# Kernel tuning notes

Measured on AMD Instinct MI355X. Metric: run time of the kernel, lower is better.

## Reference

```python
import jax, jax.numpy as jnp
import numpy as np

B, T, D, H, O, L = 32, 512, 512, 512, 2, 2


def setup_inputs() -> dict:
    key = jax.random.key(0)
    ks = jax.random.split(key, 8)
    s_in = 1.0 / np.sqrt(D + H)
    s_h = 1.0 / np.sqrt(H + H)
    x = jax.random.normal(ks[0], (B, T, D), dtype=jnp.float32)
    # Fused gate weights per layer: columns ordered [forget | input | candidate | output]
    W0 = jax.random.uniform(ks[1], (D + H, 4 * H), jnp.float32, -s_in, s_in)
    b0 = jax.random.uniform(ks[2], (4 * H,), jnp.float32, -s_in, s_in)
    W1 = jax.random.uniform(ks[3], (H + H, 4 * H), jnp.float32, -s_h, s_h)
    b1 = jax.random.uniform(ks[4], (4 * H,), jnp.float32, -s_h, s_h)
    s_r = 1.0 / np.sqrt(H)
    Wr = jax.random.uniform(ks[5], (H, O), jnp.float32, -s_r, s_r)
    br = jax.random.uniform(ks[6], (O,), jnp.float32, -s_r, s_r)
    return {"x": x, "W0": W0, "b0": b0, "W1": W1, "b1": b1, "Wr": Wr, "br": br}


def _lstm_cell(xt, h, c, W, b):
    # One fused GEMM for all 4 gates, then elementwise gate math.
    z = jnp.concatenate([xt, h], axis=1) @ W + b  # [B, 4H]
    f, i, g, o = jnp.split(z, 4, axis=1)
    new_c = c * jax.nn.sigmoid(f) + jnp.tanh(g) * jax.nn.sigmoid(i)
    # NB: original module applies tanh to the OLD cell state c (faithful to source).
    new_h = jax.nn.sigmoid(o) * jnp.tanh(c)
    return new_h, new_c


def reference(x, W0, b0, W1, b1, Wr, br):
    Bb = x.shape[0]
    zeros = jnp.zeros((Bb, H), dtype=x.dtype)

    def step(carry, xt):
        h1, c1, h2, c2 = carry
        nh1, nc1 = _lstm_cell(xt, h1, c1, W0, b0)
        nh2, nc2 = _lstm_cell(nh1, h2, c2, W1, b1)
        return (nh1, nc1, nh2, nc2), nh2

    _, ys = jax.lax.scan(step, (zeros, zeros, zeros, zeros), jnp.swapaxes(x, 0, 1))
    out = jnp.swapaxes(ys, 0, 1)  # [B, T, H]
    return out @ Wr + br  # [B, T, O]
```

## Files before the change

### kernel.cpp

```cpp
#include <hip/hip_runtime.h>
#include <hip/hip_bf16.h>
#include <stdint.h>

typedef unsigned short u16;
typedef unsigned int u32;
typedef unsigned long long u64;
typedef __attribute__((ext_vector_type(8))) short bf16x8;
typedef __attribute__((ext_vector_type(4))) float f32x4;
typedef __attribute__((ext_vector_type(4))) u32 u32x4;

#define TT 512
#define WPS ((size_t)2048 * 1024)
#define ZRS 8
#define HRS 16
#define HRS2 4

#define LD16C(dst, addr) asm volatile("global_load_dwordx4 %0, %1, off sc0 sc1" : "=v"(dst) : "v"(addr))
#define LD8C(dst, addr)  asm volatile("global_load_dwordx2 %0, %1, off sc0 sc1" : "=v"(dst) : "v"(addr))
#define LD4C(dst, addr)  asm volatile("global_load_dword %0, %1, off sc0 sc1"   : "=v"(dst) : "v"(addr))
#define ST4C(addr, v)    asm volatile("global_store_dword %0, %1, off sc0 sc1"  :: "v"(addr), "v"(v) : "memory")
#define ST8C(addr, v)    asm volatile("global_store_dwordx2 %0, %1, off sc0 sc1":: "v"(addr), "v"(v) : "memory")
#define ST16C(addr, v)   asm volatile("global_store_dwordx4 %0, %1, off sc0 sc1":: "v"(addr), "v"(v) : "memory")
#define VM0()            do { asm volatile("s_waitcnt vmcnt(0)" ::: "memory"); \
                              __builtin_amdgcn_sched_barrier(0); } while (0)

__device__ __forceinline__ u16 f2bf(float f) {
  u32 u = __builtin_bit_cast(u32, f);
  return (u16)((u + 0x7FFFu + ((u >> 16) & 1u)) >> 16);
}
__device__ __forceinline__ float bf2f(u16 h) {
  u32 u = ((u32)h) << 16;
  return __builtin_bit_cast(float, u);
}
__device__ __forceinline__ float sigm(float x) { return 1.0f / (1.0f + expf(-x)); }
__device__ __forceinline__ f32x4 mfma16(bf16x8 a, bf16x8 b, f32x4 c) {
  return __builtin_amdgcn_mfma_f32_16x16x32_bf16(a, b, c, 0, 0, 0);
}
__device__ __forceinline__ u32 cvtpk(float a, float b) {
  u32 r;
  asm volatile("v_cvt_pk_bf16_f32 %0, %1, %2" : "=v"(r) : "v"(a), "v"(b));
  return r;
}
__device__ __forceinline__ void mark_err(u32* err) {
  __hip_atomic_fetch_add(err, 1u, __ATOMIC_RELAXED, __HIP_MEMORY_SCOPE_AGENT);
}
__device__ __forceinline__ u64 pack3(float v, u32 tag) {
  u16 p0 = f2bf(v); float r1 = v - bf2f(p0);
  u16 p1 = f2bf(r1); u16 p2 = f2bf(r1 - bf2f(p1));
  return (u64)((u32)p0 | ((u32)p1 << 16)) | ((u64)((u32)p2 | (tag << 16)) << 32);
}
__device__ __forceinline__ float zval(u64 w) {
  return bf2f((u16)(w & 0xFFFFu)) + bf2f((u16)((w >> 16) & 0xFFFFu))
       + bf2f((u16)((w >> 32) & 0xFFFFu));
}

__device__ __forceinline__ void wait_slots(const u32* slots, int ln, u32 tgt,
                                           u32* lastv, int* bail, u32* err) {
  if (*bail) return;
  if (__ballot(*lastv < tgt) == 0ull) return;
  const u32* ptr = slots + (ln & 31);
  int n = 0;
  for (;;) {
    u32 v;
    LD4C(v, ptr);
    VM0();
    if (v > *lastv) *lastv = v;
    if (__ballot(*lastv < tgt) == 0ull) return;
    __builtin_amdgcn_s_sleep(2);
    if (++n > 400000) { *bail = 1; if (ln == 0) mark_err(err); return; }
  }
}

__device__ __forceinline__ void head_poll(const u64* p, u32 texp, u32* err) {
  int n = 0;
  for (;;) {
    u64 hw;
    LD8C(hw, p);
    VM0();
    if (__ballot((u32)(hw >> 48) != texp) == 0ull) return;
    __builtin_amdgcn_s_sleep(1);
    if (++n > 600000) { if ((threadIdx.x & 63) == 0) mark_err(err); return; }
  }
}

__global__ void prep_w(const float* __restrict__ W, u16* __restrict__ WT) {
  int i = blockIdx.x * 256 + threadIdx.x;
  if (i >= 2048 * 1024) return;
  int n = i >> 10, k = i & 1023;
  float v = W[(size_t)k * 2048 + n];
  u16 p0 = f2bf(v);  float r  = v - bf2f(p0);
  u16 p1 = f2bf(r);  float r2 = r - bf2f(p1);
  u16 p2 = f2bf(r2);
  size_t o = (size_t)n * 1024 + k;
  WT[o] = p0;
  WT[WPS + o] = p1;
  WT[2 * WPS + o] = p2;
}

template <int LAYER>
__device__ void chain(char* smem, int p, int bid,
                      const float* __restrict__ bias,
                      const u16* __restrict__ WT,
                      const u64* Zring, u64* hG,
                      const u32* progOther, u32* progSelf,
                      u16* h2hi, u32* err) {
  u16* wl = (u16*)smem;
  float* zl = (float*)(smem + 131072);
  const int tid = threadIdx.x;

#pragma unroll 1
  for (int it = 0; it < 32; ++it) {
    int id = it * 256 + tid;
    int pl = id >> 12, rem = id & 4095, rho = rem >> 6, m = rem & 63;
    int n = ((rho >> 4) << 9) + (bid << 4) + (rho & 15);
    u32x4 v = *(const u32x4*)(WT + (size_t)pl * WPS + (size_t)n * 1024 + 512 + m * 8);
    int dst = pl * 65536 + rho * 1024 + ((m << 4) ^ ((rho & 7) << 4));
    *(u32x4*)((char*)wl + dst) = v;
  }

  const int ln = tid & 63, kq = tid >> 6;
  const int fr = ln & 15, kg8 = (ln >> 4) << 3;
  const int row = tid >> 4, hc = tid & 15;
  float bsv[4];
#pragma unroll
  for (int g = 0; g < 4; ++g) bsv[g] = bias[(g << 9) + (bid << 4) + hc];
  const int ka = kq * 128 + kg8;
  const u16* w2base[4];
#pragma unroll
  for (int nt = 0; nt < 4; ++nt)
    w2base[nt] = WT + 2 * WPS + (size_t)((nt << 9) + (bid << 4) + fr) * 1024 + 512 + ka;
  const int hrm = (LAYER == 1) ? (HRS - 1) : (HRS2 - 1);

  float creg = 0.0f;
  u32 lastbp = 0;
  int bail = 0;
  __syncthreads();

#pragma unroll 1
  for (int t = 0; t < TT; ++t) {
    if (LAYER == 1 && kq == 0 && t >= HRS - 1)
      wait_slots(progOther, ln, (u32)(t - (HRS - 1)), &lastbp, &bail, err);

    const u64* hb = hG + (size_t)(t & hrm) * (16 * 512) + (size_t)fr * 512 + ka;
    const u64* zb = Zring + (size_t)(t & (ZRS - 1)) * (16 * 2048) + (size_t)row * 2048
                  + (bid << 4) + hc;
    const u32 texp = (u32)t, zexp = (u32)(t + 1);

    head_poll(hb, texp, err);

    u32x4 hv[4][4];
    u64 zw[4];
    int tries = 0;
    for (;;) {
#pragma unroll
      for (int kt = 0; kt < 4; ++kt)
#pragma unroll
        for (int j = 0; j < 4; ++j) LD16C(hv[kt][j], hb + kt * 32 + 2 * j);
#pragma unroll
      for (int g = 0; g < 4; ++g) LD8C(zw[g], zb + ((size_t)g << 9));
      VM0();
      u32 bad = 0;
#pragma unroll
      for (int kt = 0; kt < 4; ++kt)
#pragma unroll
        for (int j = 0; j < 4; ++j)
          bad |= ((hv[kt][j].y >> 16) ^ texp) | ((hv[kt][j].w >> 16) ^ texp);
#pragma unroll
      for (int g = 0; g < 4; ++g) bad |= ((u32)(zw[g] >> 48) ^ zexp);
      if (__ballot(bad != 0) == 0ull) break;
      if (++tries > 500000) { if (ln == 0) mark_err(err); break; }
      __builtin_amdgcn_s_sleep(1);
    }

    f32x4 acc[4] = {{0.f,0.f,0.f,0.f},{0.f,0.f,0.f,0.f},{0.f,0.f,0.f,0.f},{0.f,0.f,0.f,0.f}};
#pragma unroll
    for (int kt = 0; kt < 4; ++kt) {
      u32 r0[4], r1[4], r2[4];
#pragma unroll
      for (int j = 0; j < 4; ++j) {
        u32 lo0 = hv[kt][j].x, hi0 = hv[kt][j].y, lo1 = hv[kt][j].z, hi1 = hv[kt][j].w;
        r0[j] = (lo0 & 0xFFFFu) | (lo1 << 16);
        r1[j] = (lo0 >> 16) | (lo1 & 0xFFFF0000u);
        r2[j] = (hi0 & 0xFFFFu) | (hi1 << 16);
      }
      bf16x8 a0 = __builtin_bit_cast(bf16x8, *(u32x4*)r0);
      bf16x8 a1 = __builtin_bit_cast(bf16x8, *(u32x4*)r1);
      bf16x8 a2 = __builtin_bit_cast(bf16x8, *(u32x4*)r2);
#pragma unroll
      for (int nt = 0; nt < 4; ++nt) {
        int rho = (nt << 4) + fr;
        int kb = ((ka + kt * 32) << 1) ^ ((rho & 7) << 4);
        bf16x8 w0 = *(const bf16x8*)((char*)wl + rho * 1024 + kb);
        bf16x8 w1 = *(const bf16x8*)((char*)wl + 65536 + rho * 1024 + kb);
        bf16x8 w2 = *(const bf16x8*)(w2base[nt] + kt * 32);
        acc[nt] = mfma16(a0, w0, acc[nt]);
        acc[nt] = mfma16(a1, w0, acc[nt]);
        acc[nt] = mfma16(a2, w0, acc[nt]);
        acc[nt] = mfma16(a0, w1, acc[nt]);
        acc[nt] = mfma16(a1, w1, acc[nt]);
        acc[nt] = mfma16(a0, w2, acc[nt]);
      }
    }
    const int r4 = (ln >> 4) << 2;
    if (kq < 2) {
#pragma unroll
      for (int nt = 0; nt < 4; ++nt)
#pragma unroll
        for (int r = 0; r < 4; ++r)
          zl[(kq * 16 + r4 + r) * 66 + (nt << 4) + fr] = acc[nt][r];
    }
    __syncthreads();
    if (kq >= 2) {
#pragma unroll
      for (int nt = 0; nt < 4; ++nt)
#pragma unroll
        for (int r = 0; r < 4; ++r)
          zl[((kq - 2) * 16 + r4 + r) * 66 + (nt << 4) + fr] += acc[nt][r];
    }
    __syncthreads();

    float z4[4];
#pragma unroll
    for (int g = 0; g < 4; ++g)
      z4[g] = zl[row * 66 + (g << 4) + hc] + zl[(16 + row) * 66 + (g << 4) + hc]
            + zval(zw[g]) + bsv[g];
    float sf = sigm(z4[0]);
    float si = sigm(z4[1]);
    float tg = tanhf(z4[2]);
    float so = sigm(z4[3]);
    float hn = so * tanhf(creg);
    creg = creg * sf + tg * si;
    u64 word = pack3(hn, (u32)(t + 1));
    size_t ho = (size_t)((t + 1) & hrm) * (16 * 512) + (size_t)row * 512 + (bid << 4) + hc;
    ST8C(hG + ho, word);
    if (LAYER == 2)
      h2hi[(size_t)(t + 1) * 16384 + (size_t)(p * 16 + row) * 512 + (bid << 4) + hc] =
          (u16)(word & 0xFFFFu);
    __syncthreads();
    if (tid == 0) ST4C(progSelf + bid, (u32)(t + 1));
  }
}

__device__ void worker(char* smem, int w, const float* __restrict__ x,
                       const u16* __restrict__ W0T, const u16* __restrict__ W1T,
                       const u64* h1G, u64* Z0R, u64* ZcR,
                       const u32* prog1, const u32* prog2, u32* err) {
  const int s = w & 63, q = w >> 6;
  u16* wl1 = (u16*)smem;
  u16* wl0 = (u16*)(smem + 65536);
  float* zl = (float*)(smem + 131072);
  const int tid = threadIdx.x;

#pragma unroll 1
  for (int it = 0; it < 32; ++it) {
    int id = it * 256 + tid;
    int sl = id >> 12, rem = id & 4095, pl = rem >> 11, rem2 = rem & 2047;
    int rho = rem2 >> 6, m = rem2 & 63;
    const u16* WT = sl ? W0T : W1T;
    u32x4 v = *(const u32x4*)(WT + (size_t)pl * WPS + (size_t)(32 * s + rho) * 1024 + m * 8);
    int dst = sl * 65536 + pl * 32768 + rho * 1024 + ((m << 4) ^ ((rho & 7) << 4));
    *(u32x4*)((char*)wl1 + dst) = v;
  }

  const int ln = tid & 63, kq = tid >> 6;
  const int fr = ln & 15, kg8 = (ln >> 4) << 3;
  const int row = tid >> 4, c2 = (tid & 15) * 2;
  const int ka = kq * 128 + kg8;
  u32 last1[2] = {0, 0}, last2[2] = {0, 0}, lastbp[2] = {0, 0};
  int bail = 0;
  __syncthreads();

#pragma unroll 1
  for (int k = 0;; ++k) {
    int t = 2 * k + q;
    if (t > 511) break;

    int nz = (k < 3) ? 2 : 1;
#pragma unroll 1
    for (int e = 0; e < nz; ++e) {
      int tz = (e == 0 && k < 3) ? t : t + 6;
      if (tz > 511) continue;
#pragma unroll 1
      for (int p = 0; p < 2; ++p) {
        if (kq == 0 && tz >= ZRS)
          wait_slots(prog1 + p * 32, ln, (u32)(tz - ZRS + 1), &lastbp[p], &bail, err);
        const float* xb = x + (size_t)(p * 16 + fr) * TT * 512 + (size_t)tz * 512 + ka;
        f32x4 acc[2] = {{0.f,0.f,0.f,0.f},{0.f,0.f,0.f,0.f}};
#pragma unroll
        for (int kt = 0; kt < 4; ++kt) {
          f32x4 f0 = *(const f32x4*)(xb + kt * 32);
          f32x4 f1 = *(const f32x4*)(xb + kt * 32 + 4);
          u32 r0[4], r1[4], r2[4];
#pragma unroll
          for (int j = 0; j < 4; ++j) {
            float v0 = (j < 2) ? f0[j * 2] : f1[(j - 2) * 2];
            float v1 = (j < 2) ? f0[j * 2 + 1] : f1[(j - 2) * 2 + 1];
            u32 pk0 = cvtpk(v0, v1);
            float h0 = __builtin_bit_cast(float, pk0 << 16);
            float h1f = __builtin_bit_cast(float, pk0 & 0xFFFF0000u);
            float q0 = v0 - h0, q1 = v1 - h1f;
            u32 pk1 = cvtpk(q0, q1);
            float g0 = __builtin_bit_cast(float, pk1 << 16);
            float g1 = __builtin_bit_cast(float, pk1 & 0xFFFF0000u);
            u32 s0 = __builtin_bit_cast(u32, q0 - g0);
            u32 s1 = __builtin_bit_cast(u32, q1 - g1);
            r0[j] = pk0; r1[j] = pk1;
            r2[j] = (s0 >> 16) | (s1 & 0xFFFF0000u);
          }
          bf16x8 a0 = __builtin_bit_cast(bf16x8, *(u32x4*)r0);
          bf16x8 a1 = __builtin_bit_cast(bf16x8, *(u32x4*)r1);
          bf16x8 a2 = __builtin_bit_cast(bf16x8, *(u32x4*)r2);
#pragma unroll
          for (int nt = 0; nt < 2; ++nt) {
            int rho = (nt << 4) + fr;
            int kb = ((ka + kt * 32) << 1) ^ ((rho & 7) << 4);
            bf16x8 w0 = *(const bf16x8*)((char*)wl0 + rho * 1024 + kb);
            bf16x8 w1 = *(const bf16x8*)((char*)wl0 + 32768 + rho * 1024 + kb);
            bf16x8 w2 = *(const bf16x8*)(W0T + 2 * WPS + (size_t)(32 * s + rho) * 1024 + ka + kt * 32);
            acc[nt] = mfma16(a0, w0, acc[nt]);
            acc[nt] = mfma16(a1, w0, acc[nt]);
            acc[nt] = mfma16(a2, w0, acc[nt]);
            acc[nt] = mfma16(a0, w1, acc[nt]);
            acc[nt] = mfma16(a1, w1, acc[nt]);
            acc[nt] = mfma16(a0, w2, acc[nt]);
          }
        }
        const int r4 = (ln >> 4) << 2;
        if (kq < 2) {
#pragma unroll
          for (int nt = 0; nt < 2; ++nt)
#pragma unroll
            for (int r = 0; r < 4; ++r)
              zl[(kq * 16 + r4 + r) * 34 + (nt << 4) + fr] = acc[nt][r];
        }
        __syncthreads();
        if (kq >= 2) {
#pragma unroll
          for (int nt = 0; nt < 2; ++nt)
#pragma unroll
            for (int r = 0; r < 4; ++r)
              zl[((kq - 2) * 16 + r4 + r) * 34 + (nt << 4) + fr] += acc[nt][r];
        }
        __syncthreads();
        float v0 = zl[row * 34 + c2] + zl[(16 + row) * 34 + c2];
        float v1 = zl[row * 34 + c2 + 1] + zl[(16 + row) * 34 + c2 + 1];
        u64 w0 = pack3(v0, (u32)(tz + 1));
        u64 w1 = pack3(v1, (u32)(tz + 1));
        u32x4 st = { (u32)w0, (u32)(w0 >> 32), (u32)w1, (u32)(w1 >> 32) };
        u64* dst = Z0R + (size_t)p * ZRS * 16 * 2048 + (size_t)(tz & (ZRS - 1)) * (16 * 2048)
                 + (size_t)row * 2048 + 32 * s + c2;
        ST16C(dst, st);
        __syncthreads();
      }
    }

#pragma unroll 1
    for (int p = 0; p < 2; ++p) {
      if (kq == 0 && t >= ZRS)
        wait_slots(prog2 + p * 32, ln, (u32)(t - ZRS + 1), &last2[p], &bail, err);
      const u64* hb = h1G + (size_t)p * HRS * 16 * 512
                    + (size_t)((t + 1) & (HRS - 1)) * (16 * 512) + (size_t)fr * 512 + ka;
      const u32 texp = (u32)(t + 1);
      head_poll(hb, texp, err);
      u32x4 hv[4][4];
      int tries = 0;
      for (;;) {
#pragma unroll
        for (int kt = 0; kt < 4; ++kt)
#pragma unroll
          for (int j = 0; j < 4; ++j) LD16C(hv[kt][j], hb + kt * 32 + 2 * j);
        VM0();
        u32 bad = 0;
#pragma unroll
        for (int kt = 0; kt < 4; ++kt)
#pragma unroll
          for (int j = 0; j < 4; ++j)
            bad |= ((hv[kt][j].y >> 16) ^ texp) | ((hv[kt][j].w >> 16) ^ texp);
        if (__ballot(bad != 0) == 0ull) break;
        if (++tries > 500000) { if (ln == 0) mark_err(err); break; }
        __builtin_amdgcn_s_sleep(1);
      }
      f32x4 acc[2] = {{0.f,0.f,0.f,0.f},{0.f,0.f,0.f,0.f}};
#pragma unroll
      for (int kt = 0; kt < 4; ++kt) {
        u32 r0[4], r1[4], r2[4];
#pragma unroll
        for (int j = 0; j < 4; ++j) {
          u32 lo0 = hv[kt][j].x, hi0 = hv[kt][j].y, lo1 = hv[kt][j].z, hi1 = hv[kt][j].w;
          r0[j] = (lo0 & 0xFFFFu) | (lo1 << 16);
          r1[j] = (lo0 >> 16) | (lo1 & 0xFFFF0000u);
          r2[j] = (hi0 & 0xFFFFu) | (hi1 << 16);
        }
        bf16x8 a0 = __builtin_bit_cast(bf16x8, *(u32x4*)r0);
        bf16x8 a1 = __builtin_bit_cast(bf16x8, *(u32x4*)r1);
        bf16x8 a2 = __builtin_bit_cast(bf16x8, *(u32x4*)r2);
#pragma unroll
        for (int nt = 0; nt < 2; ++nt) {
          int rho = (nt << 4) + fr;
          int kb = ((ka + kt * 32) << 1) ^ ((rho & 7) << 4);
          bf16x8 w0 = *(const bf16x8*)((char*)wl1 + rho * 1024 + kb);
          bf16x8 w1 = *(const bf16x8*)((char*)wl1 + 32768 + rho * 1024 + kb);
          bf16x8 w2 = *(const bf16x8*)(W1T + 2 * WPS + (size_t)(32 * s + rho) * 1024 + ka + kt * 32);
          acc[nt] = mfma16(a0, w0, acc[nt]);
          acc[nt] = mfma16(a1, w0, acc[nt]);
          acc[nt] = mfma16(a2, w0, acc[nt]);
          acc[nt] = mfma16(a0, w1, acc[nt]);
          acc[nt] = mfma16(a1, w1, acc[nt]);
          acc[nt] = mfma16(a0, w2, acc[nt]);
        }
      }
      const int r4 = (ln >> 4) << 2;
      if (kq < 2) {
#pragma unroll
        for (int nt = 0; nt < 2; ++nt)
#pragma unroll
          for (int r = 0; r < 4; ++r)
            zl[(kq * 16 + r4 + r) * 34 + (nt << 4) + fr] = acc[nt][r];
      }
      __syncthreads();
      if (kq >= 2) {
#pragma unroll
        for (int nt = 0; nt < 2; ++nt)
#pragma unroll
          for (int r = 0; r < 4; ++r)
            zl[((kq - 2) * 16 + r4 + r) * 34 + (nt << 4) + fr] += acc[nt][r];
      }
      __syncthreads();
      float v0 = zl[row * 34 + c2] + zl[(16 + row) * 34 + c2];
      float v1 = zl[row * 34 + c2 + 1] + zl[(16 + row) * 34 + c2 + 1];
      u64 w0 = pack3(v0, (u32)(t + 1));
      u64 w1 = pack3(v1, (u32)(t + 1));
      u32x4 st = { (u32)w0, (u32)(w0 >> 32), (u32)w1, (u32)(w1 >> 32) };
      u64* dst = ZcR + (size_t)p * ZRS * 16 * 2048 + (size_t)(t & (ZRS - 1)) * (16 * 2048)
               + (size_t)row * 2048 + 32 * s + c2;
      ST16C(dst, st);
      __syncthreads();
    }
  }
}

__global__ void __launch_bounds__(256, 1) mega(
    const float* __restrict__ x,
    const float* __restrict__ bias0, const float* __restrict__ bias1,
    const u16* __restrict__ W0T, const u16* __restrict__ W1T,
    u64* Z0R, u64* ZcR, u64* h1G, u64* h2G, u16* h2hi, u32* flags) {
  __shared__ char smem[139520];
  const int blk = blockIdx.x;
  const int r8 = blk & 7, g8 = blk >> 3;
  u32* prog1 = flags;
  u32* prog2 = flags + 64;
  u32* err = flags + 128;
  if (r8 < 2) {
    int p = r8;
    chain<1>(smem, p, g8, bias0, W0T,
             Z0R + (size_t)p * ZRS * 16 * 2048, h1G + (size_t)p * HRS * 16 * 512,
             prog2 + p * 32, prog1 + p * 32, nullptr, err);
  } else if (r8 < 4) {
    int p = r8 - 2;
    chain<2>(smem, p, g8, bias1, W1T,
             ZcR + (size_t)p * ZRS * 16 * 2048, h2G + (size_t)p * HRS2 * 16 * 512,
             nullptr, prog2 + p * 32, h2hi, err);
  } else {
    worker(smem, (r8 - 4) * 32 + g8, x, W0T, W1T, h1G, Z0R, ZcR, prog1, prog2, err);
  }
}

__global__ void proj(const u16* __restrict__ y,
                     const float* __restrict__ Wr, const float* __restrict__ br,
                     float* __restrict__ out) {
  int gw = (blockIdx.x * blockDim.x + threadIdx.x) >> 6;
  int ln = threadIdx.x & 63;
  int t = gw >> 5, b = gw & 31;
  const u16* yp = y + (size_t)(t + 1) * 16384 + (size_t)b * 512 + ln * 8;
  u32x4 v = *(const u32x4*)yp;
  float p0 = 0.f, p1 = 0.f;
#pragma unroll
  for (int jj = 0; jj < 8; ++jj) {
    u16 hh = (u16)((v[jj >> 1] >> ((jj & 1) * 16)) & 0xFFFFu);
    float yv = bf2f(hh);
    int j = ln * 8 + jj;
    p0 += yv * Wr[j * 2 + 0];
    p1 += yv * Wr[j * 2 + 1];
  }
#pragma unroll
  for (int o = 32; o; o >>= 1) { p0 += __shfl_down(p0, o, 64); p1 += __shfl_down(p1, o, 64); }
  if (ln == 0) {
    out[((size_t)b * 512 + t) * 2 + 0] = p0 + br[0];
    out[((size_t)b * 512 + t) * 2 + 1] = p1 + br[1];
  }
}

__global__ void fail_mark(float* out, float code) {
  if (threadIdx.x == 0 && blockIdx.x == 0) out[0] = code;
}
__global__ void err_check(const u32* flags, float* out) {
  if (threadIdx.x == 0 && blockIdx.x == 0) {
    u32 e = flags[128];
    if (e) out[0] = 1.0e6f + (float)e;
  }
}

extern "C" void kernel_launch(void* const* d_in, const int* in_sizes, int n_in,
                              void* d_out, int out_size, void* d_ws, size_t ws_size,
                              hipStream_t stream) {
  (void)in_sizes; (void)n_in; (void)out_size;
  const float* x  = (const float*)d_in[0];
  const float* W0 = (const float*)d_in[1];
  const float* b0 = (const float*)d_in[2];
  const float* W1 = (const float*)d_in[3];
  const float* b1 = (const float*)d_in[4];
  const float* Wr = (const float*)d_in[5];
  const float* br = (const float*)d_in[6];
  float* out = (float*)d_out;

  char* ws = (char*)d_ws;
  size_t off = 0;
  auto take = [&](size_t n) { char* p = ws + off; off = (off + n + 255) & ~(size_t)255; return p; };

  u16* W0T  = (u16*)take(3 * WPS * 2);
  u16* W1T  = (u16*)take(3 * WPS * 2);
  u64* Z0R  = (u64*)take((size_t)2 * ZRS * 16 * 2048 * 8);
  u64* ZcR  = (u64*)take((size_t)2 * ZRS * 16 * 2048 * 8);
  u64* h1G  = (u64*)take((size_t)2 * HRS * 16 * 512 * 8);
  u64* h2G  = (u64*)take((size_t)2 * HRS2 * 16 * 512 * 8);
  u16* h2hi = (u16*)take((size_t)513 * 16384 * 2);
  u32* flags = (u32*)take(129 * 4);

  if (off > ws_size) {
    fail_mark<<<1, 1, 0, stream>>>(out, 2.0e6f);
    return;
  }

  hipMemsetAsync(flags, 0, 129 * 4, stream);
  hipMemsetAsync(Z0R, 0, (size_t)2 * ZRS * 16 * 2048 * 8, stream);
  hipMemsetAsync(ZcR, 0, (size_t)2 * ZRS * 16 * 2048 * 8, stream);
  hipMemsetAsync(h1G, 0, (size_t)2 * HRS * 16 * 512 * 8, stream);
  hipMemsetAsync(h2G, 0, (size_t)2 * HRS2 * 16 * 512 * 8, stream);

  prep_w<<<8192, 256, 0, stream>>>(W0, W0T);
  prep_w<<<8192, 256, 0, stream>>>(W1, W1T);
  (void)hipGetLastError();
  mega<<<256, 256, 0, stream>>>(x, b0, b1, W0T, W1T, Z0R, ZcR, h1G, h2G, h2hi, flags);
  if (hipGetLastError() != hipSuccess) {
    fail_mark<<<1, 1, 0, stream>>>(out, 3.0e6f);
    return;
  }
  proj<<<4096, 256, 0, stream>>>(h2hi, Wr, br, out);
  err_check<<<1, 1, 0, stream>>>(flags, out);
}
```

Baseline: 4.047 ms.

## Add XCD-local hidden-state mirror with device-scope fallback and defer Z polling

Each chain block now writes its hidden state twice: once with a device-scope store and once with an sc0-only store into a separate mirror buffer. Chain blocks in the same group poll and load from the mirror using sc0 loads, which are intended to be served from the shared L2 of the XCD instead of going device-wide. If the mirror poll times out they fall back to the device-scope copy. The Z ring load is issued before the h poll and its tag check is deferred until after the MMA reduction, taking it off the critical path. The risks are an extra store per step, correctness that depends on all blocks of a chain landing on the same XCD (the fallback handles the other case), and more complex polling logic.

```diff
diff --git a/kernel.cpp b/kernel.cpp
--- a/kernel.cpp
+++ b/kernel.cpp
@@ -18,9 +18,12 @@
 #define LD16C(dst, addr) asm volatile("global_load_dwordx4 %0, %1, off sc0 sc1" : "=v"(dst) : "v"(addr))
 #define LD8C(dst, addr)  asm volatile("global_load_dwordx2 %0, %1, off sc0 sc1" : "=v"(dst) : "v"(addr))
 #define LD4C(dst, addr)  asm volatile("global_load_dword %0, %1, off sc0 sc1"   : "=v"(dst) : "v"(addr))
+#define LD16L(dst, addr) asm volatile("global_load_dwordx4 %0, %1, off sc0"     : "=v"(dst) : "v"(addr))
+#define LD8L(dst, addr)  asm volatile("global_load_dwordx2 %0, %1, off sc0"     : "=v"(dst) : "v"(addr))
 #define ST4C(addr, v)    asm volatile("global_store_dword %0, %1, off sc0 sc1"  :: "v"(addr), "v"(v) : "memory")
 #define ST8C(addr, v)    asm volatile("global_store_dwordx2 %0, %1, off sc0 sc1":: "v"(addr), "v"(v) : "memory")
 #define ST16C(addr, v)   asm volatile("global_store_dwordx4 %0, %1, off sc0 sc1":: "v"(addr), "v"(v) : "memory")
+#define ST8L(addr, v)    asm volatile("global_store_dwordx2 %0, %1, off"        :: "v"(addr), "v"(v) : "memory")
 #define VM0()            do { asm volatile("s_waitcnt vmcnt(0)" ::: "memory"); \
                               __builtin_amdgcn_sched_barrier(0); } while (0)
 
@@ -101,7 +104,7 @@
 __device__ void chain(char* smem, int p, int bid,
                       const float* __restrict__ bias,
                       const u16* __restrict__ WT,
-                      const u64* Zring, u64* hG,
+                      const u64* Zring, u64* hL, u64* hG,
                       const u32* progOther, u32* progSelf,
                       u16* h2hi, u32* err) {
   u16* wl = (u16*)smem;
@@ -130,10 +133,12 @@
   for (int nt = 0; nt < 4; ++nt)
     w2base[nt] = WT + 2 * WPS + (size_t)((nt << 9) + (bid << 4) + fr) * 1024 + 512 + ka;
   const int hrm = (LAYER == 1) ? (HRS - 1) : (HRS2 - 1);
+  const int pcol = ((ln >> 1) << 4) + ((ln & 1) << 9);
 
   float creg = 0.0f;
   u32 lastbp = 0;
   int bail = 0;
+  int useG = 0;
   __syncthreads();
 
 #pragma unroll 1
@@ -141,23 +146,44 @@
     if (LAYER == 1 && kq == 0 && t >= HRS - 1)
       wait_slots(progOther, ln, (u32)(t - (HRS - 1)), &lastbp, &bail, err);
 
-    const u64* hb = hG + (size_t)(t & hrm) * (16 * 512) + (size_t)fr * 512 + ka;
+    const size_t soff = (size_t)(t & hrm) * (16 * 512);
+    const u64* hbL = hL + soff + (size_t)fr * 512 + ka;
+    const u64* hbG = hG + soff + (size_t)fr * 512 + ka;
     const u64* zb = Zring + (size_t)(t & (ZRS - 1)) * (16 * 2048) + (size_t)row * 2048
                   + (bid << 4) + hc;
     const u32 texp = (u32)t, zexp = (u32)(t + 1);
 
-    head_poll(hb, texp, err);
+    u64 zw[4];
+#pragma unroll
+    for (int g = 0; g < 4; ++g) LD8C(zw[g], zb + ((size_t)g << 9));
+
+    if (!useG) {
+      int n = 0;
+      for (;;) {
+        u64 hw;
+        LD8L(hw, hL + soff + pcol);
+        VM0();
+        if (__ballot((u32)(hw >> 48) != texp) == 0ull) break;
+        __builtin_amdgcn_s_sleep(1);
+        if (++n > 4000) { useG = 1; break; }
+      }
+    }
+    if (useG) head_poll(hG + soff + pcol, texp, err);
 
     u32x4 hv[4][4];
-    u64 zw[4];
     int tries = 0;
     for (;;) {
-#pragma unroll
-      for (int kt = 0; kt < 4; ++kt)
-#pragma unroll
-        for (int j = 0; j < 4; ++j) LD16C(hv[kt][j], hb + kt * 32 + 2 * j);
-#pragma unroll
-      for (int g = 0; g < 4; ++g) LD8C(zw[g], zb + ((size_t)g << 9));
+      if (!useG) {
+#pragma unroll
+        for (int kt = 0; kt < 4; ++kt)
+#pragma unroll
+          for (int j = 0; j < 4; ++j) LD16L(hv[kt][j], hbL + kt * 32 + 2 * j);
+      } else {
+#pragma unroll
+        for (int kt = 0; kt < 4; ++kt)
+#pragma unroll
+          for (int j = 0; j < 4; ++j) LD16C(hv[kt][j], hbG + kt * 32 + 2 * j);
+      }
       VM0();
       u32 bad = 0;
 #pragma unroll
@@ -165,10 +191,10 @@
 #pragma unroll
         for (int j = 0; j < 4; ++j)
           bad |= ((hv[kt][j].y >> 16) ^ texp) | ((hv[kt][j].w >> 16) ^ texp);
-#pragma unroll
-      for (int g = 0; g < 4; ++g) bad |= ((u32)(zw[g] >> 48) ^ zexp);
       if (__ballot(bad != 0) == 0ull) break;
-      if (++tries > 500000) { if (ln == 0) mark_err(err); break; }
+      ++tries;
+      if (tries == 64 && !useG) useG = 1;
+      if (tries > 500000) { if (ln == 0) mark_err(err); break; }
       __builtin_amdgcn_s_sleep(1);
     }
 
@@ -219,6 +245,18 @@
     }
     __syncthreads();
 
+    int ztries = 0;
+    for (;;) {
+      u32 zbad = 0;
+#pragma unroll
+      for (int g = 0; g < 4; ++g) zbad |= ((u32)(zw[g] >> 48) ^ zexp);
+      if (__ballot(zbad != 0) == 0ull) break;
+      __builtin_amdgcn_s_sleep(1);
+#pragma unroll
+      for (int g = 0; g < 4; ++g) LD8C(zw[g], zb + ((size_t)g << 9));
+      VM0();
+      if (++ztries > 500000) { if (ln == 0) mark_err(err); break; }
+    }
     float z4[4];
 #pragma unroll
     for (int g = 0; g < 4; ++g)
@@ -227,11 +265,12 @@
     float sf = sigm(z4[0]);
     float si = sigm(z4[1]);
     float tg = tanhf(z4[2]);
-    float so = sigm(z4[3]);
-    float hn = so * tanhf(creg);
+    float sog = sigm(z4[3]);
+    float hn = sog * tanhf(creg);
     creg = creg * sf + tg * si;
     u64 word = pack3(hn, (u32)(t + 1));
     size_t ho = (size_t)((t + 1) & hrm) * (16 * 512) + (size_t)row * 512 + (bid << 4) + hc;
+    ST8L(hL + ho, word);
     ST8C(hG + ho, word);
     if (LAYER == 2)
       h2hi[(size_t)(t + 1) * 16384 + (size_t)(p * 16 + row) * 512 + (bid << 4) + hc] =
@@ -266,7 +305,8 @@
   const int fr = ln & 15, kg8 = (ln >> 4) << 3;
   const int row = tid >> 4, c2 = (tid & 15) * 2;
   const int ka = kq * 128 + kg8;
-  u32 last1[2] = {0, 0}, last2[2] = {0, 0}, lastbp[2] = {0, 0};
+  const int pcol = ((ln >> 1) << 4) + ((ln & 1) << 9);
+  u32 last2[2] = {0, 0}, lastbp[2] = {0, 0};
   int bail = 0;
   __syncthreads();
 
@@ -358,10 +398,10 @@
     for (int p = 0; p < 2; ++p) {
       if (kq == 0 && t >= ZRS)
         wait_slots(prog2 + p * 32, ln, (u32)(t - ZRS + 1), &last2[p], &bail, err);
-      const u64* hb = h1G + (size_t)p * HRS * 16 * 512
-                    + (size_t)((t + 1) & (HRS - 1)) * (16 * 512) + (size_t)fr * 512 + ka;
+      const size_t sb = (size_t)p * HRS * 16 * 512 + (size_t)((t + 1) & (HRS - 1)) * (16 * 512);
+      const u64* hb = h1G + sb + (size_t)fr * 512 + ka;
       const u32 texp = (u32)(t + 1);
-      head_poll(hb, texp, err);
+      head_poll(h1G + sb + pcol, texp, err);
       u32x4 hv[4][4];
       int tries = 0;
       for (;;) {
@@ -443,7 +483,8 @@
     const float* __restrict__ x,
     const float* __restrict__ bias0, const float* __restrict__ bias1,
     const u16* __restrict__ W0T, const u16* __restrict__ W1T,
-    u64* Z0R, u64* ZcR, u64* h1G, u64* h2G, u16* h2hi, u32* flags) {
+    u64* Z0R, u64* ZcR, u64* h1L, u64* h1G, u64* h2L, u64* h2G,
+    u16* h2hi, u32* flags) {
   __shared__ char smem[139520];
   const int blk = blockIdx.x;
   const int r8 = blk & 7, g8 = blk >> 3;
@@ -453,12 +494,14 @@
   if (r8 < 2) {
     int p = r8;
     chain<1>(smem, p, g8, bias0, W0T,
-             Z0R + (size_t)p * ZRS * 16 * 2048, h1G + (size_t)p * HRS * 16 * 512,
+             Z0R + (size_t)p * ZRS * 16 * 2048,
+             h1L + (size_t)p * HRS * 16 * 512, h1G + (size_t)p * HRS * 16 * 512,
              prog2 + p * 32, prog1 + p * 32, nullptr, err);
   } else if (r8 < 4) {
     int p = r8 - 2;
     chain<2>(smem, p, g8, bias1, W1T,
-             ZcR + (size_t)p * ZRS * 16 * 2048, h2G + (size_t)p * HRS2 * 16 * 512,
+             ZcR + (size_t)p * ZRS * 16 * 2048,
+             h2L + (size_t)p * HRS2 * 16 * 512, h2G + (size_t)p * HRS2 * 16 * 512,
              nullptr, prog2 + p * 32, h2hi, err);
   } else {
     worker(smem, (r8 - 4) * 32 + g8, x, W0T, W1T, h1G, Z0R, ZcR, prog1, prog2, err);
@@ -521,7 +564,9 @@
   u16* W1T  = (u16*)take(3 * WPS * 2);
   u64* Z0R  = (u64*)take((size_t)2 * ZRS * 16 * 2048 * 8);
   u64* ZcR  = (u64*)take((size_t)2 * ZRS * 16 * 2048 * 8);
+  u64* h1L  = (u64*)take((size_t)2 * HRS * 16 * 512 * 8);
   u64* h1G  = (u64*)take((size_t)2 * HRS * 16 * 512 * 8);
+  u64* h2L  = (u64*)take((size_t)2 * HRS2 * 16 * 512 * 8);
   u64* h2G  = (u64*)take((size_t)2 * HRS2 * 16 * 512 * 8);
   u16* h2hi = (u16*)take((size_t)513 * 16384 * 2);
   u32* flags = (u32*)take(129 * 4);
@@ -531,16 +576,19 @@
     return;
   }
 
-  hipMemsetAsync(flags, 0, 129 * 4, stream);
-  hipMemsetAsync(Z0R, 0, (size_t)2 * ZRS * 16 * 2048 * 8, stream);
-  hipMemsetAsync(ZcR, 0, (size_t)2 * ZRS * 16 * 2048 * 8, stream);
-  hipMemsetAsync(h1G, 0, (size_t)2 * HRS * 16 * 512 * 8, stream);
-  hipMemsetAsync(h2G, 0, (size_t)2 * HRS2 * 16 * 512 * 8, stream);
+  (void)hipMemsetAsync(flags, 0, 129 * 4, stream);
+  (void)hipMemsetAsync(Z0R, 0, (size_t)2 * ZRS * 16 * 2048 * 8, stream);
+  (void)hipMemsetAsync(ZcR, 0, (size_t)2 * ZRS * 16 * 2048 * 8, stream);
+  (void)hipMemsetAsync(h1L, 0, (size_t)2 * HRS * 16 * 512 * 8, stream);
+  (void)hipMemsetAsync(h1G, 0, (size_t)2 * HRS * 16 * 512 * 8, stream);
+  (void)hipMemsetAsync(h2L, 0, (size_t)2 * HRS2 * 16 * 512 * 8, stream);
+  (void)hipMemsetAsync(h2G, 0, (size_t)2 * HRS2 * 16 * 512 * 8, stream);
 
   prep_w<<<8192, 256, 0, stream>>>(W0, W0T);
   prep_w<<<8192, 256, 0, stream>>>(W1, W1T);
   (void)hipGetLastError();
-  mega<<<256, 256, 0, stream>>>(x, b0, b1, W0T, W1T, Z0R, ZcR, h1G, h2G, h2hi, flags);
+  mega<<<256, 256, 0, stream>>>(x, b0, b1, W0T, W1T,
+                                Z0R, ZcR, h1L, h1G, h2L, h2G, h2hi, flags);
   if (hipGetLastError() != hipSuccess) {
     fail_mark<<<1, 1, 0, stream>>>(out, 3.0e6f);
     return;
```

New measurement: 5.136 ms. +26.9%, slower.
